# Performance work log

Hardware: AMD Instinct MI355X
Metric: run time of the kernel (lower is better)

Reference implementation:

```python
import jax, jax.numpy as jnp
import numpy as np
from jax import lax

T, E, H = 4096, 1024, 1024


def setup_inputs() -> dict:
    key = jax.random.key(0)
    ks = jax.random.split(key, 14)
    u = lambda k, shp: jax.random.uniform(k, shp, dtype=jnp.float32) * 0.02  # small so gates don't saturate
    return {
        "x": jax.random.normal(ks[0], (T, E), dtype=jnp.float32),
        "Uf": u(ks[1], (H, E)), "Wf": u(ks[2], (H, H)), "Bf": u(ks[3], (H,)),
        "Ug": u(ks[4], (H, E)), "Wg": u(ks[5], (H, H)), "Bg": u(ks[6], (H,)),
        "Uq": u(ks[7], (H, E)), "Wq": u(ks[8], (H, H)), "Bq": u(ks[9], (H,)),
        "U": u(ks[10], (H, E)), "W": u(ks[11], (H, H)), "B": u(ks[12], (H,)),
    }


def reference(x, Uf, Wf, Bf, Ug, Wg, Bg, Uq, Wq, Bq, U, W, B):
    hdim = Wf.shape[0]
    # Precompute all input projections in 4 big GEMMs: [T, H] each
    xf = x @ Uf.T + Bf
    xc = x @ U.T + B
    xg = x @ Ug.T + Bg
    xq = x @ Uq.T + Bq

    def step(carry, inp):
        h, s = carry
        xf_t, xc_t, xg_t, xq_t = inp
        f = jax.nn.sigmoid(Wf @ h + xf_t)
        c = jax.nn.sigmoid(W @ h + xc_t)   # note: original uses sigmoid (not tanh) for the candidate
        g = jax.nn.sigmoid(Wg @ h + xg_t)
        s = f * s + g * c
        q = jax.nn.sigmoid(Wq @ h + xq_t)
        h = jnp.tanh(s) * q
        return (h, s), h

    init = (jnp.zeros((hdim,), x.dtype), jnp.zeros((hdim,), x.dtype))
    _, out = lax.scan(step, init, (xf, xc, xg, xq))
    return out  # [T, H]
```

## Files before the change

kernel.cpp:

```cpp
#include <hip/hip_runtime.h>
#include <hip/hip_fp16.h>
#include <stdint.h>


#define T_STEPS 4096
#define HDIM 1024

typedef _Float16 half2v __attribute__((ext_vector_type(2)));

__device__ __forceinline__ float dot2(uint32_t a, uint32_t b, float c) {
#if __has_builtin(__builtin_amdgcn_fdot2)
  return __builtin_amdgcn_fdot2(__builtin_bit_cast(half2v, a),
                                __builtin_bit_cast(half2v, b), c, false);
#else
  half2v av = __builtin_bit_cast(half2v, a);
  half2v bv = __builtin_bit_cast(half2v, b);
  return c + (float)av.x * (float)bv.x + (float)av.y * (float)bv.y;
#endif
}

__global__ __launch_bounds__(256) void convw(const float* __restrict__ w0,
                                             const float* __restrict__ w1,
                                             const float* __restrict__ w2,
                                             const float* __restrict__ w3,
                                             __half* __restrict__ dst) {
  int i = (blockIdx.x * 256 + threadIdx.x) * 4;
  int g = i >> 20;
  int off = i & 1048575;
  const float* src = g == 0 ? w0 : g == 1 ? w1 : g == 2 ? w2 : w3;
  float4 v = *(const float4*)(src + off);
  union { __half h[4]; uint2 u; } cv;
  cv.h[0] = __float2half(v.x); cv.h[1] = __float2half(v.y);
  cv.h[2] = __float2half(v.z); cv.h[3] = __float2half(v.w);
  *(uint2*)(dst + i) = cv.u;
}

__global__ void zerok(uint32_t* __restrict__ p) {
  int i = blockIdx.x * 256 + threadIdx.x;
  if (i < 2048) p[i] = 0;
}

__global__ __launch_bounds__(256) void gemmk(
    const float* __restrict__ x,
    const float* __restrict__ u0, const float* __restrict__ u1,
    const float* __restrict__ u2, const float* __restrict__ u3,
    const float* __restrict__ b0, const float* __restrict__ b1,
    const float* __restrict__ b2, const float* __restrict__ b3,
    __half* __restrict__ xpre) {
  __shared__ float As[64][33];
  __shared__ float Bs[64][33];
  const int tid = threadIdx.x;
  const int m0 = blockIdx.y * 64;
  const int n0 = blockIdx.x * 64;
  const int g = n0 >> 10;
  const float* Up = g == 0 ? u0 : g == 1 ? u1 : g == 2 ? u2 : u3;
  const float* Bp = g == 0 ? b0 : g == 1 ? b1 : g == 2 ? b2 : b3;
  const int j0 = n0 & 1023;
  const int tx = tid & 15, ty = tid >> 4;
  const int lr = tid >> 3, lc = (tid & 7) << 2;
  float acc[4][4] = {};
  for (int k0 = 0; k0 < 1024; k0 += 32) {
    float4 a0 = *(const float4*)&x[(size_t)(m0 + lr) * 1024 + k0 + lc];
    float4 a1 = *(const float4*)&x[(size_t)(m0 + lr + 32) * 1024 + k0 + lc];
    float4 c0 = *(const float4*)&Up[(size_t)(j0 + lr) * 1024 + k0 + lc];
    float4 c1 = *(const float4*)&Up[(size_t)(j0 + lr + 32) * 1024 + k0 + lc];
    __syncthreads();
    As[lr][lc + 0] = a0.x; As[lr][lc + 1] = a0.y; As[lr][lc + 2] = a0.z; As[lr][lc + 3] = a0.w;
    As[lr + 32][lc + 0] = a1.x; As[lr + 32][lc + 1] = a1.y; As[lr + 32][lc + 2] = a1.z; As[lr + 32][lc + 3] = a1.w;
    Bs[lr][lc + 0] = c0.x; Bs[lr][lc + 1] = c0.y; Bs[lr][lc + 2] = c0.z; Bs[lr][lc + 3] = c0.w;
    Bs[lr + 32][lc + 0] = c1.x; Bs[lr + 32][lc + 1] = c1.y; Bs[lr + 32][lc + 2] = c1.z; Bs[lr + 32][lc + 3] = c1.w;
    __syncthreads();
#pragma unroll
    for (int k = 0; k < 32; ++k) {
      float a0v = As[ty * 4 + 0][k], a1v = As[ty * 4 + 1][k];
      float a2v = As[ty * 4 + 2][k], a3v = As[ty * 4 + 3][k];
      float b0v = Bs[tx * 4 + 0][k], b1v = Bs[tx * 4 + 1][k];
      float b2v = Bs[tx * 4 + 2][k], b3v = Bs[tx * 4 + 3][k];
      acc[0][0] += a0v * b0v; acc[0][1] += a0v * b1v; acc[0][2] += a0v * b2v; acc[0][3] += a0v * b3v;
      acc[1][0] += a1v * b0v; acc[1][1] += a1v * b1v; acc[1][2] += a1v * b2v; acc[1][3] += a1v * b3v;
      acc[2][0] += a2v * b0v; acc[2][1] += a2v * b1v; acc[2][2] += a2v * b2v; acc[2][3] += a2v * b3v;
      acc[3][0] += a3v * b0v; acc[3][1] += a3v * b1v; acc[3][2] += a3v * b2v; acc[3][3] += a3v * b3v;
    }
  }
#pragma unroll
  for (int i = 0; i < 4; ++i) {
    size_t rowi = (size_t)(m0 + ty * 4 + i);
#pragma unroll
    for (int j = 0; j < 4; ++j) {
      int jj = j0 + tx * 4 + j;
      float v = acc[i][j] + Bp[jj];
      xpre[rowi * 4096 + n0 + tx * 4 + j] = __float2half(v);
    }
  }
}

__global__ __launch_bounds__(512, 2) void rnnk(
    const __half* __restrict__ w16,
    const __half* __restrict__ xpre,
    uint32_t* tagged,
    float* __restrict__ out) {
  __shared__ uint32_t hl[4 * 136];
  __shared__ float gl[128];
  const int wg = blockIdx.x;
  const int tid = threadIdx.x;
  const int wave = tid >> 6, lane = tid & 63;
  const int g = wave >> 1;
  const int rloc = ((wave & 1) << 4) + (lane >> 2);
  const int row = (wg << 5) + rloc;
  const int c = lane & 3;
  const bool rowlead = (c == 0);
  const bool w0 = (wave == 0);

  uint4 wreg[32];
  {
    const uint4* wp = reinterpret_cast<const uint4*>(
        w16 + ((size_t)g << 20) + ((size_t)row << 10) + (c << 8));
#pragma unroll
    for (int i = 0; i < 32; ++i) wreg[i] = wp[i];
  }

  float s = 0.f;

  for (int t = 0; t < T_STEPS; ++t) {
    float xv = 0.f;
    if (rowlead)
      xv = __half2float(xpre[(size_t)t * 4096 + ((size_t)g << 10) + row]);

    {
      const unsigned long long* pp =
          reinterpret_cast<const unsigned long long*>(tagged + ((t & 1) << 10)) + tid;
      const uint32_t tg = (uint32_t)t;
      unsigned long long v =
          __hip_atomic_load(pp, __ATOMIC_RELAXED, __HIP_MEMORY_SCOPE_AGENT);
      while ((((uint32_t)(v >> 16) & 0xffffu) != tg) ||
             (((uint32_t)(v >> 48) & 0xffffu) != tg)) {
        __builtin_amdgcn_s_sleep(1);
        v = __hip_atomic_load(pp, __ATOMIC_RELAXED, __HIP_MEMORY_SCOPE_AGENT);
      }
      uint32_t pair = (uint32_t)(v & 0xffffu) | (((uint32_t)(v >> 32) & 0xffffu) << 16);
      hl[(tid >> 7) * 136 + (tid & 127)] = pair;
    }
    __syncthreads();

    float p = 0.f;
    const uint4* hp = reinterpret_cast<const uint4*>(&hl[c * 136]);
#pragma unroll
    for (int i = 0; i < 32; ++i) {
      uint4 h4 = hp[i];
      p = dot2(wreg[i].x, h4.x, p);
      p = dot2(wreg[i].y, h4.y, p);
      p = dot2(wreg[i].z, h4.z, p);
      p = dot2(wreg[i].w, h4.w, p);
    }
    p += __shfl_xor(p, 1);
    p += __shfl_xor(p, 2);

    if (rowlead) {
      float z = p + xv;
      gl[(g << 5) + rloc] = 1.f / (1.f + __expf(-z));
    }
    __syncthreads();

    if (w0 && lane < 32) {
      const int r = lane;
      float f = gl[r], cc = gl[32 + r], gg = gl[64 + r], q = gl[96 + r];
      s = f * s + gg * cc;
      float e2 = __expf(2.f * s);
      float th = 1.f - 2.f / (e2 + 1.f);
      float h = th * q;
      out[(size_t)t * HDIM + (wg << 5) + r] = h;
      uint32_t hb = (uint32_t)__half_as_ushort(__float2half(h));
      uint32_t dw = ((uint32_t)(t + 1) << 16) | hb;
      __hip_atomic_store(&tagged[(((t + 1) & 1) << 10) + (wg << 5) + r], dw,
                         __ATOMIC_RELAXED, __HIP_MEMORY_SCOPE_AGENT);
    }
  }
}

extern "C" void kernel_launch(void* const* d_in, const int* in_sizes, int n_in,
                              void* d_out, int out_size, void* d_ws, size_t ws_size,
                              hipStream_t stream) {
  const float* x  = (const float*)d_in[0];
  const float* Uf = (const float*)d_in[1];
  const float* Wf = (const float*)d_in[2];
  const float* Bf = (const float*)d_in[3];
  const float* Ug = (const float*)d_in[4];
  const float* Wg = (const float*)d_in[5];
  const float* Bg = (const float*)d_in[6];
  const float* Uq = (const float*)d_in[7];
  const float* Wq = (const float*)d_in[8];
  const float* Bq = (const float*)d_in[9];
  const float* U  = (const float*)d_in[10];
  const float* W  = (const float*)d_in[11];
  const float* B  = (const float*)d_in[12];
  float* out = (float*)d_out;

  char* ws = (char*)d_ws;
  __half* xpre = (__half*)ws;
  __half* w16 = (__half*)(ws + (size_t)32 * 1024 * 1024);
  uint32_t* tagged = (uint32_t*)(ws + (size_t)40 * 1024 * 1024);

  convw<<<4096, 256, 0, stream>>>(Wf, W, Wg, Wq, w16);
  zerok<<<8, 256, 0, stream>>>(tagged);
  gemmk<<<dim3(64, 64), 256, 0, stream>>>(x, Uf, U, Ug, Uq, Bf, B, Bg, Bq, xpre);
  rnnk<<<32, 512, 0, stream>>>(w16, xpre, tagged, out);
}
```

Measured before the change: 7.695 ms.

## Poll recurrent state with one wave and pin weights in VGPRs

```diff
diff --git a/kernel.cpp b/kernel.cpp
--- a/kernel.cpp
+++ b/kernel.cpp
@@ -99,7 +99,7 @@
     const __half* __restrict__ xpre,
     uint32_t* tagged,
     float* __restrict__ out) {
-  __shared__ uint32_t hl[4 * 136];
+  __shared__ uint32_t hl[4 * 132];
   __shared__ float gl[128];
   const int wg = blockIdx.x;
   const int tid = threadIdx.x;
@@ -111,13 +111,19 @@
   const bool rowlead = (c == 0);
   const bool w0 = (wave == 0);
 
-  uint4 wreg[32];
+  uint32_t wv[128];
   {
     const uint4* wp = reinterpret_cast<const uint4*>(
         w16 + ((size_t)g << 20) + ((size_t)row << 10) + (c << 8));
 #pragma unroll
-    for (int i = 0; i < 32; ++i) wreg[i] = wp[i];
-  }
+    for (int i = 0; i < 32; ++i) {
+      uint4 w4 = wp[i];
+      wv[4 * i + 0] = w4.x; wv[4 * i + 1] = w4.y;
+      wv[4 * i + 2] = w4.z; wv[4 * i + 3] = w4.w;
+    }
+  }
+#pragma unroll
+  for (int j = 0; j < 128; ++j) asm volatile("" : "+v"(wv[j]));
 
   float s = 0.f;
 
@@ -126,31 +132,44 @@
     if (rowlead)
       xv = __half2float(xpre[(size_t)t * 4096 + ((size_t)g << 10) + row]);
 
-    {
+    if (w0) {
       const unsigned long long* pp =
-          reinterpret_cast<const unsigned long long*>(tagged + ((t & 1) << 10)) + tid;
+          reinterpret_cast<const unsigned long long*>(tagged + ((t & 1) << 10)) +
+          (lane << 3);
       const uint32_t tg = (uint32_t)t;
-      unsigned long long v =
-          __hip_atomic_load(pp, __ATOMIC_RELAXED, __HIP_MEMORY_SCOPE_AGENT);
-      while ((((uint32_t)(v >> 16) & 0xffffu) != tg) ||
-             (((uint32_t)(v >> 48) & 0xffffu) != tg)) {
-        __builtin_amdgcn_s_sleep(1);
-        v = __hip_atomic_load(pp, __ATOMIC_RELAXED, __HIP_MEMORY_SCOPE_AGENT);
-      }
-      uint32_t pair = (uint32_t)(v & 0xffffu) | (((uint32_t)(v >> 32) & 0xffffu) << 16);
-      hl[(tid >> 7) * 136 + (tid & 127)] = pair;
+      unsigned long long v[8];
+      bool ok;
+      do {
+#pragma unroll
+        for (int j = 0; j < 8; ++j)
+          v[j] = __hip_atomic_load(pp + j, __ATOMIC_RELAXED, __HIP_MEMORY_SCOPE_AGENT);
+        ok = true;
+#pragma unroll
+        for (int j = 0; j < 8; ++j)
+          ok = ok && (((uint32_t)(v[j] >> 16) & 0xffffu) == tg) &&
+               (((uint32_t)(v[j] >> 48) & 0xffffu) == tg);
+      } while (!ok);
+      uint32_t pk[8];
+#pragma unroll
+      for (int j = 0; j < 8; ++j)
+        pk[j] = (uint32_t)(v[j] & 0xffffu) | (((uint32_t)(v[j] >> 32) & 0xffffu) << 16);
+      uint32_t* dst = &hl[132 * (lane >> 4) + ((lane << 3) & 127)];
+      uint4 w1; w1.x = pk[0]; w1.y = pk[1]; w1.z = pk[2]; w1.w = pk[3];
+      uint4 w2; w2.x = pk[4]; w2.y = pk[5]; w2.z = pk[6]; w2.w = pk[7];
+      *reinterpret_cast<uint4*>(dst) = w1;
+      *reinterpret_cast<uint4*>(dst + 4) = w2;
     }
     __syncthreads();
 
     float p = 0.f;
-    const uint4* hp = reinterpret_cast<const uint4*>(&hl[c * 136]);
+    const uint4* hp = reinterpret_cast<const uint4*>(&hl[132 * c]);
 #pragma unroll
     for (int i = 0; i < 32; ++i) {
       uint4 h4 = hp[i];
-      p = dot2(wreg[i].x, h4.x, p);
-      p = dot2(wreg[i].y, h4.y, p);
-      p = dot2(wreg[i].z, h4.z, p);
-      p = dot2(wreg[i].w, h4.w, p);
+      p = dot2(wv[4 * i + 0], h4.x, p);
+      p = dot2(wv[4 * i + 1], h4.y, p);
+      p = dot2(wv[4 * i + 2], h4.z, p);
+      p = dot2(wv[4 * i + 3], h4.w, p);
     }
     p += __shfl_xor(p, 1);
     p += __shfl_xor(p, 2);
```

After: 8.900 ms. 1.16x slower.
